# Optimization experiments

Hardware: AMD Instinct MI355X
Metric: run time of the kernel (lower is better)

The kernel has to match this reference:

```python
import jax, jax.numpy as jnp
import numpy as np

B, T, H, W, C = 2, 8, 64, 64, 192
WIN = (4, 8, 8)
SHIFT = (2, 4, 4)
HEADS = 6
HID = 4 * C
N = WIN[0] * WIN[1] * WIN[2]  # 256 tokens per window
CPB_HID = 512


def window_partition(x, win):
    b, t, h, w, c = x.shape
    x = x.reshape(b, t // win[0], win[0], h // win[1], win[1], w // win[2], win[2], c)
    x = x.transpose(0, 1, 3, 5, 2, 4, 6, 7)
    return x.reshape(-1, win[0] * win[1] * win[2], c)


def window_reverse(wins, win, b, t, h, w):
    x = wins.reshape(b, t // win[0], h // win[1], w // win[2], win[0], win[1], win[2], -1)
    x = x.transpose(0, 1, 4, 2, 5, 3, 6, 7)
    return x.reshape(b, t, h, w, -1)


def _rel_coords_table():
    axes = [np.arange(-(WIN[i] - 1), WIN[i], dtype=np.float32) for i in range(3)]
    tbl = np.stack(np.meshgrid(*axes, indexing='ij'), axis=-1)  # (2wt-1,2wh-1,2ww-1,3)
    for i in range(3):
        tbl[..., i] /= WIN[i] - 1
    tbl *= 8.0
    tbl = np.sign(tbl) * np.log2(np.abs(tbl) + 1.0) / np.log2(8.0)
    return tbl.reshape(-1, 3)


def _rel_pos_index():
    coords = np.stack(np.meshgrid(np.arange(WIN[0]), np.arange(WIN[1]), np.arange(WIN[2]), indexing='ij'))
    cf = coords.reshape(3, -1)
    rel = (cf[:, :, None] - cf[:, None, :]).transpose(1, 2, 0)
    rel[..., 0] += WIN[0] - 1
    rel[..., 1] += WIN[1] - 1
    rel[..., 2] += WIN[2] - 1
    rel[..., 0] *= (2 * WIN[1] - 1) * (2 * WIN[2] - 1)
    rel[..., 1] *= 2 * WIN[2] - 1
    return rel.sum(-1)  # (N, N) int


def _attn_mask():
    img = np.zeros((1, T, H, W, 1), dtype=np.float32)
    cnt = 0
    for d in (slice(-WIN[0]), slice(-WIN[0], -SHIFT[0]), slice(-SHIFT[0], None)):
        for h in (slice(-WIN[1]), slice(-WIN[1], -SHIFT[1]), slice(-SHIFT[1], None)):
            for w in (slice(-WIN[2]), slice(-WIN[2], -SHIFT[2]), slice(-SHIFT[2], None)):
                img[:, d, h, w, :] = cnt
                cnt += 1
    mw = window_partition(img, WIN).squeeze(-1)  # (nW, N)
    am = mw[:, None, :] - mw[:, :, None]
    return np.where(am != 0, -100.0, 0.0).astype(np.float32)


REL_TABLE = jnp.asarray(_rel_coords_table())      # (M, 3)
RPI = jnp.asarray(_rel_pos_index().reshape(-1))   # (N*N,)
MASK = jnp.asarray(_attn_mask())                  # (nW, N, N)


def _ln(x, g, b):
    m = x.mean(-1, keepdims=True)
    v = x.var(-1, keepdims=True)
    return (x - m) / jnp.sqrt(v + 1e-5) * g + b


def setup_inputs() -> dict:
    key = jax.random.key(0)
    ks = jax.random.split(key, 16)
    s = lambda fan: 1.0 / np.sqrt(fan)
    return {
        'x': jax.random.normal(ks[0], (B, T, H, W, C), jnp.float32),
        'qkv_w': jax.random.normal(ks[1], (3 * C, C), jnp.float32) * s(C),
        'qkv_b': jnp.zeros((3 * C,), jnp.float32),
        'proj_w': jax.random.normal(ks[2], (C, C), jnp.float32) * s(C),
        'proj_b': jnp.zeros((C,), jnp.float32),
        'cpb_w1': jax.random.normal(ks[3], (CPB_HID, 3), jnp.float32) * s(3),
        'cpb_b1': jnp.zeros((CPB_HID,), jnp.float32),
        'cpb_w2': jax.random.normal(ks[4], (HEADS, CPB_HID), jnp.float32) * s(CPB_HID),
        'logit_scale': jnp.log(10.0 * jnp.ones((HEADS, 1, 1), jnp.float32)),
        'norm1_g': jnp.ones((C,), jnp.float32),
        'norm1_b': jnp.zeros((C,), jnp.float32),
        'norm2_g': jnp.ones((C,), jnp.float32),
        'norm2_b': jnp.zeros((C,), jnp.float32),
        'fc1_w': jax.random.normal(ks[5], (HID, C), jnp.float32) * s(C),
        'fc1_b': jnp.zeros((HID,), jnp.float32),
        'fc2_w': jax.random.normal(ks[6], (C, HID), jnp.float32) * s(HID),
        'fc2_b': jnp.zeros((C,), jnp.float32),
    }


def reference(x, qkv_w, qkv_b, proj_w, proj_b, cpb_w1, cpb_b1, cpb_w2,
              logit_scale, norm1_g, norm1_b, norm2_g, norm2_b,
              fc1_w, fc1_b, fc2_w, fc2_b):
    shortcut = x
    # cyclic shift
    xs = jnp.roll(x, shift=(-SHIFT[0], -SHIFT[1], -SHIFT[2]), axis=(1, 2, 3))
    xw = window_partition(xs, WIN)  # (B*nW, N, C)
    B_ = xw.shape[0]
    d = C // HEADS
    qkv = (xw @ qkv_w.T + qkv_b).reshape(B_, N, 3, HEADS, d).transpose(2, 0, 3, 1, 4)
    q, k, v = qkv[0], qkv[1], qkv[2]  # (B_, h, N, d)
    # cosine attention (F.normalize eps=1e-12)
    qn = q / jnp.maximum(jnp.linalg.norm(q, axis=-1, keepdims=True), 1e-12)
    kn = k / jnp.maximum(jnp.linalg.norm(k, axis=-1, keepdims=True), 1e-12)
    attn = jnp.einsum('bhnd,bhmd->bhnm', qn, kn)
    scale = jnp.exp(jnp.minimum(logit_scale, jnp.log(100.0)))  # clamp at log(1/0.01)
    attn = attn * scale
    # continuous relative position bias
    tbl = jax.nn.relu(REL_TABLE @ cpb_w1.T + cpb_b1) @ cpb_w2.T  # (M, heads)
    bias = tbl[RPI].reshape(N, N, HEADS).transpose(2, 0, 1)      # (h, N, N)
    attn = attn + 16.0 * jax.nn.sigmoid(bias)[None]
    # shift mask
    nW = MASK.shape[0]
    attn = attn.reshape(B_ // nW, nW, HEADS, N, N) + MASK[None, :, None]
    attn = jax.nn.softmax(attn.reshape(B_, HEADS, N, N), axis=-1)
    out = jnp.einsum('bhnm,bhmd->bhnd', attn, v)
    out = out.transpose(0, 2, 1, 3).reshape(B_, N, C)
    out = out @ proj_w.T + proj_b
    xr = window_reverse(out, WIN, B, T, H, W)
    xr = jnp.roll(xr, shift=SHIFT, axis=(1, 2, 3))
    # SwinV2 res-post-norm residual
    x = shortcut + _ln(xr, norm1_g, norm1_b)
    h1 = jax.nn.gelu(x @ fc1_w.T + fc1_b, approximate=False)
    x = x + _ln(h1 @ fc2_w.T + fc2_b, norm2_g, norm2_b)
    return x
```

## Files before the change

### kernel.cpp

```cpp
#include <hip/hip_runtime.h>
#include <math.h>


typedef short short8 __attribute__((ext_vector_type(8)));
typedef short short4v __attribute__((ext_vector_type(4)));
typedef float f32x4 __attribute__((ext_vector_type(4)));

__device__ __forceinline__ short f2bf(float f) {
    union { float f; unsigned u; } v; v.f = f;
    unsigned r = v.u + 0x7FFF + ((v.u >> 16) & 1);
    return (short)(r >> 16);
}
__device__ __forceinline__ short f2h(float f) {
    _Float16 h = (_Float16)f;
    union { _Float16 h; short s; } u; u.h = h; return u.s;
}
__device__ __forceinline__ float h2f(short s) {
    union { _Float16 h; short s; } u; u.s = s; return (float)u.h;
}

__device__ __forceinline__ float gelu_fast(float x) {
    float s = x * x;
    float t = fmaf(0.044715f, s, 1.0f);
    float y = -1.5957691216057308f * x * t;
    return x * __builtin_amdgcn_rcpf(1.0f + __expf(y));
}

__global__ __launch_bounds__(64) void pack_w_k(const float* __restrict__ w,
                                               short* __restrict__ dst, int K) {
    int lane = threadIdx.x;
    int ktn = K >> 5;
    int nt = blockIdx.x / ktn, kt = blockIdx.x % ktn;
    int r = lane & 15, q = lane >> 4;
    const float* src = w + (size_t)(nt * 16 + r) * K + kt * 32 + q * 8;
    short8 v;
#pragma unroll
    for (int j = 0; j < 8; j++) v[j] = f2bf(src[j]);
    ((short8*)dst)[(size_t)blockIdx.x * 64 + lane] = v;
}

__global__ __launch_bounds__(64) void cpb_table_k(const float* __restrict__ w1,
                                                  const float* __restrict__ b1,
                                                  const float* __restrict__ w2,
                                                  float* __restrict__ tbl6) {
    int m = blockIdx.x;
    int lane = threadIdx.x;
    int it = m / 225;
    int ih = (m / 15) % 15;
    int iw = m % 15;
    float r0 = (float)(it - 3) * (8.0f / 3.0f);
    float r1 = (float)(ih - 7) * (8.0f / 7.0f);
    float r2 = (float)(iw - 7) * (8.0f / 7.0f);
    float c0 = (r0 < 0.f ? -1.f : 1.f) * log2f(fabsf(r0) + 1.0f) * (1.0f / 3.0f);
    float c1 = (r1 < 0.f ? -1.f : 1.f) * log2f(fabsf(r1) + 1.0f) * (1.0f / 3.0f);
    float c2 = (r2 < 0.f ? -1.f : 1.f) * log2f(fabsf(r2) + 1.0f) * (1.0f / 3.0f);
    float hv[8];
#pragma unroll
    for (int j = 0; j < 8; j++) {
        int t = lane * 8 + j;
        hv[j] = fmaxf(0.0f, c0 * w1[3 * t] + c1 * w1[3 * t + 1] + c2 * w1[3 * t + 2] + b1[t]);
    }
#pragma unroll
    for (int head = 0; head < 6; head++) {
        float s = 0.f;
#pragma unroll
        for (int j = 0; j < 8; j++) s += hv[j] * w2[head * 512 + lane * 8 + j];
        s += __shfl_xor(s, 1);
        s += __shfl_xor(s, 2);
        s += __shfl_xor(s, 4);
        s += __shfl_xor(s, 8);
        s += __shfl_xor(s, 16);
        s += __shfl_xor(s, 32);
        if (lane == 0) tbl6[m * 6 + head] = s;
    }
}

__global__ __launch_bounds__(256) void bias_k(const float* __restrict__ tbl6,
                                              short* __restrict__ biasPK) {
    int idx = blockIdx.x * 256 + threadIdx.x;
    int kh = idx & 1;
    int query = (idx >> 1) & 255;
    int r = (idx >> 9) & 15;
    int s = (idx >> 13) & 7;
    int h = idx >> 16;
    int key = s * 32 + kh * 16 + r;
    int dt = (query >> 6) - (key >> 6) + 3;
    int dh = ((query >> 3) & 7) - ((key >> 3) & 7) + 7;
    int dw = (query & 7) - (key & 7) + 7;
    int rel = dt * 225 + dh * 15 + dw;
    float v = tbl6[rel * 6 + h];
    biasPK[idx] = f2h(16.0f / (1.0f + expf(-v)));
}

#define ZSTR 388
__global__ __launch_bounds__(256) void qkv_mfma_k(const float* __restrict__ x,
                                                  const short* __restrict__ wqp,
                                                  const float* __restrict__ qkv_b,
                                                  short* __restrict__ qbf,
                                                  short* __restrict__ kbf,
                                                  short* __restrict__ vtb) {
    __shared__ float Z[32 * ZSTR];
    int tid = threadIdx.x, lane = tid & 63, w = tid >> 6;
    int r = lane & 15, q = lane >> 4;
    int b_ = blockIdx.x >> 3, n0 = (blockIdx.x & 7) << 5;
    int b = b_ >> 7, win = b_ & 127;
    int wt = win >> 6, wh = (win >> 3) & 7, ww = win & 7;

    short8 af[2][6];
#pragma unroll
    for (int m = 0; m < 2; m++) {
        int n = n0 + m * 16 + r;
        int t0 = ((wt * 4 + (n >> 6)) + 2) & 7;
        int h0 = ((wh * 8 + ((n >> 3) & 7)) + 4) & 63;
        int w0 = ((ww * 8 + (n & 7)) + 4) & 63;
        const float* src = x + ((size_t)((b * 8 + t0) * 64 + h0) * 64 + w0) * 192 + q * 8;
#pragma unroll
        for (int kt = 0; kt < 6; kt++) {
            float4 x0 = *(const float4*)(src + kt * 32);
            float4 x1 = *(const float4*)(src + kt * 32 + 4);
            short8 v;
            v[0] = f2bf(x0.x); v[1] = f2bf(x0.y); v[2] = f2bf(x0.z); v[3] = f2bf(x0.w);
            v[4] = f2bf(x1.x); v[5] = f2bf(x1.y); v[6] = f2bf(x1.z); v[7] = f2bf(x1.w);
            af[m][kt] = v;
        }
    }

    for (int ntl = 0; ntl < 9; ntl++) {
        int nt = w * 9 + ntl;
        float bias = qkv_b[nt * 16 + r];
        short8 bfr[6];
#pragma unroll
        for (int kt = 0; kt < 6; kt++)
            bfr[kt] = ((const short8*)wqp)[(size_t)(nt * 6 + kt) * 64 + lane];
        f32x4 a0 = {bias, bias, bias, bias};
        f32x4 a1 = {bias, bias, bias, bias};
#pragma unroll
        for (int kt = 0; kt < 6; kt++) {
            a0 = __builtin_amdgcn_mfma_f32_16x16x32_bf16(af[0][kt], bfr[kt], a0, 0, 0, 0);
            a1 = __builtin_amdgcn_mfma_f32_16x16x32_bf16(af[1][kt], bfr[kt], a1, 0, 0, 0);
        }
        int col = nt * 16 + r;
        if (nt < 24) {
#pragma unroll
            for (int reg = 0; reg < 4; reg++) {
                Z[(q * 4 + reg) * ZSTR + col] = a0[reg];
                Z[(16 + q * 4 + reg) * ZSTR + col] = a1[reg];
            }
        } else {
            int ch = col - 384;
            int hh = ch >> 5, dd = ch & 31;
            short* vb = vtb + ((size_t)(b_ * 6 + hh) * 32 + dd) * 256 + n0;
            short4v p0, p1;
#pragma unroll
            for (int reg = 0; reg < 4; reg++) { p0[reg] = f2bf(a0[reg]); p1[reg] = f2bf(a1[reg]); }
            *(short4v*)(vb + q * 4) = p0;
            *(short4v*)(vb + 16 + q * 4) = p1;
        }
    }
    __syncthreads();
    for (int rw = tid; rw < 384; rw += 256) {
        int token = rw / 12, rr = rw - token * 12;
        int isq = rr < 6 ? 1 : 0;
        int h = isq ? rr : rr - 6;
        const float* rp = &Z[token * ZSTR + rr * 32];
        float ss = 0.f;
#pragma unroll
        for (int d4 = 0; d4 < 8; d4++) {
            f32x4 v4 = *(const f32x4*)(rp + d4 * 4);
            ss += v4[0] * v4[0] + v4[1] * v4[1] + v4[2] * v4[2] + v4[3] * v4[3];
        }
        float inv = 1.0f / fmaxf(sqrtf(ss), 1e-12f);
        short* dst = (isq ? qbf : kbf) + ((size_t)(b_ * 6 + h) * 256 + n0 + token) * 32;
#pragma unroll
        for (int d8 = 0; d8 < 4; d8++) {
            f32x4 a4 = *(const f32x4*)(rp + d8 * 8);
            f32x4 b4 = *(const f32x4*)(rp + d8 * 8 + 4);
            short8 v;
            v[0] = f2bf(a4[0] * inv); v[1] = f2bf(a4[1] * inv);
            v[2] = f2bf(a4[2] * inv); v[3] = f2bf(a4[3] * inv);
            v[4] = f2bf(b4[0] * inv); v[5] = f2bf(b4[1] * inv);
            v[6] = f2bf(b4[2] * inv); v[7] = f2bf(b4[3] * inv);
            *(short8*)(dst + d8 * 8) = v;
        }
    }
}

#define KSTR 40
#define VSTR 264
#define PSTR 40
__global__ __launch_bounds__(256) void attn_mfma_k(const short* __restrict__ qbf,
                                                   const short* __restrict__ kbf,
                                                   const short* __restrict__ vtb,
                                                   const short* __restrict__ biasPK,
                                                   const float* __restrict__ logit_scale,
                                                   short* __restrict__ att) {
    __shared__ short Ks[256 * KSTR];
    __shared__ short Vs[32 * VSTR];
    __shared__ short Ps[4][16 * PSTR];
    int tid = threadIdx.x, lane = tid & 63, w = tid >> 6;
    int r = lane & 15, q = lane >> 4;
    int b_ = blockIdx.x / 6, h = blockIdx.x % 6;
    size_t base = (size_t)(b_ * 6 + h) * 8192;

    const short8* kg = (const short8*)(kbf + base);
    const short8* vg = (const short8*)(vtb + base);
    for (int i = tid; i < 1024; i += 256) {
        short8 kv = kg[i];
        *(short8*)&Ks[(i >> 2) * KSTR + (i & 3) * 8] = kv;
        short8 vv = vg[i];
        *(short8*)&Vs[(i >> 5) * VSTR + (i & 31) * 8] = vv;
    }

    short8 qf[4];
#pragma unroll
    for (int mt = 0; mt < 4; mt++)
        qf[mt] = *(const short8*)(qbf + base + (size_t)(w * 64 + mt * 16 + r) * 32 + q * 8);

    float scale = __expf(fminf(logit_scale[h], 4.6051702f));
    float M = scale + 16.0f;
    int win = b_ & 127;
    int wt4 = (win >> 6) * 4, wh8 = ((win >> 3) & 7) * 8, ww8 = (win & 7) * 8;
    auto region = [&](int n) {
        int ts = wt4 + (n >> 6), hs = wh8 + ((n >> 3) & 7), wsv = ww8 + (n & 7);
        int rt = ts < 4 ? 0 : (ts < 6 ? 1 : 2);
        int rh = hs < 56 ? 0 : (hs < 60 ? 1 : 2);
        int rw = wsv < 56 ? 0 : (wsv < 60 ? 1 : 2);
        return rt * 9 + rh * 3 + rw;
    };
    int rowreg[4][4];
#pragma unroll
    for (int mt = 0; mt < 4; mt++)
#pragma unroll
        for (int reg = 0; reg < 4; reg++)
            rowreg[mt][reg] = region(w * 64 + mt * 16 + q * 4 + reg);

    f32x4 O[4][2];
    float lp[4][4];
#pragma unroll
    for (int mt = 0; mt < 4; mt++) {
        O[mt][0] = (f32x4){0.f, 0.f, 0.f, 0.f};
        O[mt][1] = (f32x4){0.f, 0.f, 0.f, 0.f};
#pragma unroll
        for (int reg = 0; reg < 4; reg++) lp[mt][reg] = 0.f;
    }
    __syncthreads();

    const short* bh = biasPK + ((size_t)h << 16);
    for (int s = 0; s < 8; s++) {
        short8 kf0 = *(const short8*)&Ks[(s * 32 + r) * KSTR + q * 8];
        short8 kf1 = *(const short8*)&Ks[(s * 32 + 16 + r) * KSTR + q * 8];
        short8 vf0 = *(const short8*)&Vs[r * VSTR + s * 32 + q * 8];
        short8 vf1 = *(const short8*)&Vs[(16 + r) * VSTR + s * 32 + q * 8];
        int cr0 = region(s * 32 + r);
        int cr1 = region(s * 32 + 16 + r);
#pragma unroll
        for (int mt = 0; mt < 4; mt++) {
            f32x4 s0 = {0.f, 0.f, 0.f, 0.f};
            f32x4 s1 = {0.f, 0.f, 0.f, 0.f};
            s0 = __builtin_amdgcn_mfma_f32_16x16x32_bf16(qf[mt], kf0, s0, 0, 0, 0);
            s1 = __builtin_amdgcn_mfma_f32_16x16x32_bf16(qf[mt], kf1, s1, 0, 0, 0);
            int qcol = w * 64 + mt * 16 + q * 4;
            short8 bv = *(const short8*)(bh + (size_t)(s * 16 + r) * 512 + qcol * 2);
#pragma unroll
            for (int reg = 0; reg < 4; reg++) {
                float bb0 = h2f(bv[2 * reg]);
                float bb1 = h2f(bv[2 * reg + 1]);
                float v0 = s0[reg] * scale + bb0 + (cr0 == rowreg[mt][reg] ? 0.f : -100.f) - M;
                float v1 = s1[reg] * scale + bb1 + (cr1 == rowreg[mt][reg] ? 0.f : -100.f) - M;
                float p0 = __expf(v0);
                float p1 = __expf(v1);
                lp[mt][reg] += p0 + p1;
                Ps[w][(q * 4 + reg) * PSTR + r] = f2bf(p0);
                Ps[w][(q * 4 + reg) * PSTR + 16 + r] = f2bf(p1);
            }
            short8 pa = *(const short8*)&Ps[w][r * PSTR + q * 8];
            O[mt][0] = __builtin_amdgcn_mfma_f32_16x16x32_bf16(vf0, pa, O[mt][0], 0, 0, 0);
            O[mt][1] = __builtin_amdgcn_mfma_f32_16x16x32_bf16(vf1, pa, O[mt][1], 0, 0, 0);
        }
    }

#pragma unroll
    for (int mt = 0; mt < 4; mt++)
#pragma unroll
        for (int reg = 0; reg < 4; reg++) {
            float v = lp[mt][reg];
            v += __shfl_xor(v, 1);
            v += __shfl_xor(v, 2);
            v += __shfl_xor(v, 4);
            v += __shfl_xor(v, 8);
            lp[mt][reg] = 1.0f / v;
        }
#pragma unroll
    for (int mt = 0; mt < 4; mt++) {
        int srcl = (r >> 2) << 4;
        float t0 = __shfl(lp[mt][0], srcl);
        float t1 = __shfl(lp[mt][1], srcl);
        float t2 = __shfl(lp[mt][2], srcl);
        float t3 = __shfl(lp[mt][3], srcl);
        int rm = r & 3;
        float linv = rm == 0 ? t0 : (rm == 1 ? t1 : (rm == 2 ? t2 : t3));
        int query = w * 64 + mt * 16 + r;
        short* dst = att + ((size_t)b_ * 256 + query) * 192 + h * 32 + q * 4;
#pragma unroll
        for (int nt = 0; nt < 2; nt++) {
            short4v pv;
#pragma unroll
            for (int reg = 0; reg < 4; reg++) pv[reg] = f2bf(O[mt][nt][reg] * linv);
            *(short4v*)(dst + nt * 16) = pv;
        }
    }
}

__global__ __launch_bounds__(256) void proj_mfma_k(const short* __restrict__ att,
                                                   const short* __restrict__ wpp,
                                                   const float* __restrict__ proj_b,
                                                   const float* __restrict__ x,
                                                   const float* __restrict__ g1,
                                                   const float* __restrict__ b1n,
                                                   float* __restrict__ out,
                                                   short* __restrict__ xmb) {
    __shared__ float ps[32][4], pss[32][4];
    __shared__ float mean_s[32], inv_s[32];
    int tid = threadIdx.x, lane = tid & 63, w = tid >> 6;
    int r = lane & 15, q = lane >> 4;
    int b_ = blockIdx.x >> 3, n0 = (blockIdx.x & 7) << 5;

    short8 af[2][6];
#pragma unroll
    for (int m = 0; m < 2; m++) {
        const short* src = att + ((size_t)b_ * 256 + n0 + m * 16 + r) * 192 + q * 8;
#pragma unroll
        for (int kt = 0; kt < 6; kt++)
            af[m][kt] = *(const short8*)(src + kt * 32);
    }
    f32x4 acc[3][2];
#pragma unroll
    for (int ntl = 0; ntl < 3; ntl++) {
        int nt = w * 3 + ntl;
        f32x4 binit = *(const f32x4*)(proj_b + nt * 16 + q * 4);
        short8 bfr[6];
#pragma unroll
        for (int kt = 0; kt < 6; kt++)
            bfr[kt] = ((const short8*)wpp)[(size_t)(nt * 6 + kt) * 64 + lane];
        f32x4 a0 = binit, a1 = binit;
#pragma unroll
        for (int kt = 0; kt < 6; kt++) {
            a0 = __builtin_amdgcn_mfma_f32_16x16x32_bf16(bfr[kt], af[0][kt], a0, 0, 0, 0);
            a1 = __builtin_amdgcn_mfma_f32_16x16x32_bf16(bfr[kt], af[1][kt], a1, 0, 0, 0);
        }
        acc[ntl][0] = a0;
        acc[ntl][1] = a1;
    }
    float s0 = 0.f, ss0 = 0.f, s1 = 0.f, ss1 = 0.f;
#pragma unroll
    for (int ntl = 0; ntl < 3; ntl++)
#pragma unroll
        for (int reg = 0; reg < 4; reg++) {
            float z0 = acc[ntl][0][reg], z1 = acc[ntl][1][reg];
            s0 += z0; ss0 += z0 * z0;
            s1 += z1; ss1 += z1 * z1;
        }
    s0 += __shfl_xor(s0, 16); ss0 += __shfl_xor(ss0, 16);
    s0 += __shfl_xor(s0, 32); ss0 += __shfl_xor(ss0, 32);
    s1 += __shfl_xor(s1, 16); ss1 += __shfl_xor(ss1, 16);
    s1 += __shfl_xor(s1, 32); ss1 += __shfl_xor(ss1, 32);
    if (q == 0) {
        ps[r][w] = s0;  pss[r][w] = ss0;
        ps[16 + r][w] = s1;  pss[16 + r][w] = ss1;
    }
    __syncthreads();
    if (tid < 32) {
        float sm = ps[tid][0] + ps[tid][1] + ps[tid][2] + ps[tid][3];
        float sq = pss[tid][0] + pss[tid][1] + pss[tid][2] + pss[tid][3];
        float mean = sm * (1.0f / 192.0f);
        float var = sq * (1.0f / 192.0f) - mean * mean;
        mean_s[tid] = mean;
        inv_s[tid] = 1.0f / sqrtf(var + 1e-5f);
    }
    __syncthreads();
    int b = b_ >> 7, win = b_ & 127;
    int wt = win >> 6, wh = (win >> 3) & 7, ww = win & 7;
#pragma unroll
    for (int mh = 0; mh < 2; mh++) {
        int token = mh * 16 + r;
        int n = n0 + token;
        int t0 = ((wt * 4 + (n >> 6)) + 2) & 7;
        int h0 = ((wh * 8 + ((n >> 3) & 7)) + 4) & 63;
        int w0 = ((ww * 8 + (n & 7)) + 4) & 63;
        size_t gb = ((size_t)((b * 8 + t0) * 64 + h0) * 64 + w0) * 192;
        float mean = mean_s[token], inv = inv_s[token];
#pragma unroll
        for (int ntl = 0; ntl < 3; ntl++) {
            int ch = (w * 3 + ntl) * 16 + q * 4;
            f32x4 zv = acc[ntl][mh];
            f32x4 gv = *(const f32x4*)(g1 + ch);
            f32x4 bv = *(const f32x4*)(b1n + ch);
            f32x4 xv = *(const f32x4*)(x + gb + ch);
            f32x4 o;
            short4v xm;
#pragma unroll
            for (int j = 0; j < 4; j++) {
                o[j] = xv[j] + (zv[j] - mean) * inv * gv[j] + bv[j];
                xm[j] = f2bf(o[j]);
            }
            *(f32x4*)(out + gb + ch) = o;
            *(short4v*)(xmb + gb + ch) = xm;
        }
    }
}

#define XSTR 204
#define H2STR 268
__global__ __launch_bounds__(512, 4) void mlp_mfma_k(const short* __restrict__ xmb,
                                                     const short* __restrict__ w1p,
                                                     const short* __restrict__ w2p,
                                                     const float* __restrict__ fc1_b,
                                                     const float* __restrict__ fc2_b,
                                                     const float* __restrict__ g2,
                                                     const float* __restrict__ b2,
                                                     float* __restrict__ out) {
    __shared__ short Xs[64 * XSTR];
    __shared__ short Hs[64 * H2STR];
    __shared__ float ps[64][4], pss[64][4];
    __shared__ float mean_s[64], inv_s[64];
    int tid = threadIdx.x;
    int lane = tid & 63, w = tid >> 6;
    int r = lane & 15, q = lane >> 4;
    size_t tok0 = (size_t)blockIdx.x * 64;

    for (int i = tid; i < 1536; i += 512) {
        int token = i / 24, ch8 = (i - token * 24) * 8;
        short8 v = *(const short8*)(xmb + (tok0 + token) * 192 + ch8);
        *(short8*)&Xs[token * XSTR + ch8] = v;
    }
    __syncthreads();

    int mg = w >> 2;
    int ng = w & 3;
    f32x4 acc2[6];
#pragma unroll
    for (int i = 0; i < 6; i++) acc2[i] = (f32x4){0.f, 0.f, 0.f, 0.f};

    for (int c = 0; c < 3; c++) {
        {
            int ntg0 = c * 16 + 2 * w;
            f32x4 a[2][4];
#pragma unroll
            for (int ntl = 0; ntl < 2; ntl++) {
                f32x4 binit = *(const f32x4*)(fc1_b + (ntg0 + ntl) * 16 + q * 4);
#pragma unroll
                for (int m = 0; m < 4; m++) a[ntl][m] = binit;
            }
#pragma unroll
            for (int kt = 0; kt < 6; kt++) {
                short8 w0 = ((const short8*)w1p)[(size_t)((ntg0) * 6 + kt) * 64 + lane];
                short8 w1f = ((const short8*)w1p)[(size_t)((ntg0 + 1) * 6 + kt) * 64 + lane];
                short8 xb[4];
#pragma unroll
                for (int m = 0; m < 4; m++)
                    xb[m] = *(const short8*)&Xs[(m * 16 + r) * XSTR + kt * 32 + q * 8];
#pragma unroll
                for (int m = 0; m < 4; m++) {
                    a[0][m] = __builtin_amdgcn_mfma_f32_16x16x32_bf16(w0, xb[m], a[0][m], 0, 0, 0);
                    a[1][m] = __builtin_amdgcn_mfma_f32_16x16x32_bf16(w1f, xb[m], a[1][m], 0, 0, 0);
                }
            }
#pragma unroll
            for (int ntl = 0; ntl < 2; ntl++) {
                int hcol = (2 * w + ntl) * 16 + q * 4;
#pragma unroll
                for (int m = 0; m < 4; m++) {
                    short4v p;
#pragma unroll
                    for (int reg = 0; reg < 4; reg++) p[reg] = f2bf(gelu_fast(a[ntl][m][reg]));
                    *(short4v*)&Hs[(m * 16 + r) * H2STR + hcol] = p;
                }
            }
        }
        __syncthreads();

#pragma unroll
        for (int kk = 0; kk < 8; kk++) {
            short8 hb0 = *(const short8*)&Hs[((mg * 2) * 16 + r) * H2STR + kk * 32 + q * 8];
            short8 hb1 = *(const short8*)&Hs[((mg * 2 + 1) * 16 + r) * H2STR + kk * 32 + q * 8];
            int kkg = c * 8 + kk;
#pragma unroll
            for (int n = 0; n < 3; n++) {
                int ntz = ng * 3 + n;
                short8 wf = ((const short8*)w2p)[(size_t)(ntz * 24 + kkg) * 64 + lane];
                acc2[n * 2 + 0] = __builtin_amdgcn_mfma_f32_16x16x32_bf16(wf, hb0, acc2[n * 2 + 0], 0, 0, 0);
                acc2[n * 2 + 1] = __builtin_amdgcn_mfma_f32_16x16x32_bf16(wf, hb1, acc2[n * 2 + 1], 0, 0, 0);
            }
        }
        __syncthreads();
    }

    float s0 = 0.f, ss0 = 0.f, s1 = 0.f, ss1 = 0.f;
#pragma unroll
    for (int n = 0; n < 3; n++) {
        f32x4 b4 = *(const f32x4*)(fc2_b + (ng * 3 + n) * 16 + q * 4);
        f32x4 z0 = acc2[n * 2 + 0] + b4;
        f32x4 z1 = acc2[n * 2 + 1] + b4;
        acc2[n * 2 + 0] = z0;
        acc2[n * 2 + 1] = z1;
#pragma unroll
        for (int reg = 0; reg < 4; reg++) {
            s0 += z0[reg]; ss0 += z0[reg] * z0[reg];
            s1 += z1[reg]; ss1 += z1[reg] * z1[reg];
        }
    }
    s0 += __shfl_xor(s0, 16); ss0 += __shfl_xor(ss0, 16);
    s0 += __shfl_xor(s0, 32); ss0 += __shfl_xor(ss0, 32);
    s1 += __shfl_xor(s1, 16); ss1 += __shfl_xor(ss1, 16);
    s1 += __shfl_xor(s1, 32); ss1 += __shfl_xor(ss1, 32);
    if (q == 0) {
        int t0 = mg * 32 + r;
        ps[t0][ng] = s0;  pss[t0][ng] = ss0;
        ps[t0 + 16][ng] = s1;  pss[t0 + 16][ng] = ss1;
    }
    __syncthreads();
    if (tid < 64) {
        float sm = ps[tid][0] + ps[tid][1] + ps[tid][2] + ps[tid][3];
        float sq = pss[tid][0] + pss[tid][1] + pss[tid][2] + pss[tid][3];
        float mean = sm * (1.0f / 192.0f);
        float var = sq * (1.0f / 192.0f) - mean * mean;
        mean_s[tid] = mean;
        inv_s[tid] = 1.0f / sqrtf(var + 1e-5f);
    }
    __syncthreads();
#pragma unroll
    for (int n = 0; n < 3; n++) {
        int ntz = ng * 3 + n;
        f32x4 g4 = *(const f32x4*)(g2 + ntz * 16 + q * 4);
        f32x4 bb4 = *(const f32x4*)(b2 + ntz * 16 + q * 4);
#pragma unroll
        for (int mh = 0; mh < 2; mh++) {
            int token = mg * 32 + mh * 16 + r;
            float mean = mean_s[token], inv = inv_s[token];
            size_t gi = (tok0 + token) * 192 + ntz * 16 + q * 4;
            f32x4 o = *(const f32x4*)(out + gi);
            f32x4 z = acc2[n * 2 + mh];
            f32x4 res;
#pragma unroll
            for (int reg = 0; reg < 4; reg++)
                res[reg] = o[reg] + (z[reg] - mean) * inv * g4[reg] + bb4[reg];
            *(f32x4*)(out + gi) = res;
        }
    }
}

extern "C" void kernel_launch(void* const* d_in, const int* in_sizes, int n_in,
                              void* d_out, int out_size, void* d_ws, size_t ws_size,
                              hipStream_t stream) {
    const float* x           = (const float*)d_in[0];
    const float* qkv_w       = (const float*)d_in[1];
    const float* qkv_b       = (const float*)d_in[2];
    const float* proj_w      = (const float*)d_in[3];
    const float* proj_b      = (const float*)d_in[4];
    const float* cpb_w1      = (const float*)d_in[5];
    const float* cpb_b1      = (const float*)d_in[6];
    const float* cpb_w2      = (const float*)d_in[7];
    const float* logit_scale = (const float*)d_in[8];
    const float* norm1_g     = (const float*)d_in[9];
    const float* norm1_b     = (const float*)d_in[10];
    const float* norm2_g     = (const float*)d_in[11];
    const float* norm2_b     = (const float*)d_in[12];
    const float* fc1_w       = (const float*)d_in[13];
    const float* fc1_b       = (const float*)d_in[14];
    const float* fc2_w       = (const float*)d_in[15];
    const float* fc2_b       = (const float*)d_in[16];
    float* out = (float*)d_out;

    float* ws = (float*)d_ws;
    const size_t QKVE = (size_t)256 * 6 * 256 * 32;
    short* att    = (short*)ws;
    short* biasPK = (short*)(ws + QKVE);
    float* tbl6   = ws + QKVE + (size_t)6 * 256 * 256;
    short* w1pack = (short*)(tbl6 + 9472);
    short* w2pack = w1pack + (size_t)768 * 192;
    short* wqpack = w2pack + (size_t)192 * 768;
    short* wppack = wqpack + (size_t)576 * 192;
    short* qbf    = wppack + (size_t)192 * 192;
    short* kbf    = qbf + QKVE;
    short* vtb    = kbf + QKVE;
    short* xmb    = vtb + QKVE;

    hipLaunchKernelGGL(pack_w_k, dim3(288), dim3(64), 0, stream, fc1_w, w1pack, 192);
    hipLaunchKernelGGL(pack_w_k, dim3(288), dim3(64), 0, stream, fc2_w, w2pack, 768);
    hipLaunchKernelGGL(pack_w_k, dim3(216), dim3(64), 0, stream, qkv_w, wqpack, 192);
    hipLaunchKernelGGL(pack_w_k, dim3(72), dim3(64), 0, stream, proj_w, wppack, 192);
    hipLaunchKernelGGL(cpb_table_k, dim3(1575), dim3(64), 0, stream, cpb_w1, cpb_b1, cpb_w2, tbl6);
    hipLaunchKernelGGL(bias_k, dim3(1536), dim3(256), 0, stream, tbl6, biasPK);
    hipLaunchKernelGGL(qkv_mfma_k, dim3(2048), dim3(256), 0, stream, x, wqpack, qkv_b, qbf, kbf, vtb);
    hipLaunchKernelGGL(attn_mfma_k, dim3(1536), dim3(256), 0, stream, qbf, kbf, vtb, biasPK, logit_scale, att);
    hipLaunchKernelGGL(proj_mfma_k, dim3(2048), dim3(256), 0, stream, att, wppack, proj_b, x, norm1_g, norm1_b, out, xmb);
    hipLaunchKernelGGL(mlp_mfma_k, dim3(1024), dim3(512), 0, stream, xmb, w1pack, w2pack,
                       fc1_b, fc2_b, norm2_g, norm2_b, out);
}
```

Before: 367.7 us.

## Compute transposed attention scores and pass probabilities via shuffles instead of LDS

The attention kernel now computes S^T (keys as rows) by swapping the MFMA operands and feeds the bf16-packed probabilities to the PV MFMA through lane shuffles, dropping the per-wave LDS round trip for P. The bias table is re-laid out query-major so each lane does one contiguous 16-byte load, and the shift-mask region checks are computed per key block from precomputed components. The row-sum reduction is simplified to two xor shuffles. Separately, the MLP kernel's LDS row strides are changed, which may alter bank-conflict behaviour.

```diff
diff --git a/kernel.cpp b/kernel.cpp
--- a/kernel.cpp
+++ b/kernel.cpp
@@ -10,6 +10,9 @@
     union { float f; unsigned u; } v; v.f = f;
     unsigned r = v.u + 0x7FFF + ((v.u >> 16) & 1);
     return (short)(r >> 16);
+}
+__device__ __forceinline__ unsigned pk2bf(float lo, float hi) {
+    return ((unsigned)(unsigned short)f2bf(lo)) | (((unsigned)(unsigned short)f2bf(hi)) << 16);
 }
 __device__ __forceinline__ short f2h(float f) {
     _Float16 h = (_Float16)f;
@@ -76,20 +79,20 @@
 }
 
 __global__ __launch_bounds__(256) void bias_k(const float* __restrict__ tbl6,
-                                              short* __restrict__ biasPK) {
+                                              short* __restrict__ biasQK) {
     int idx = blockIdx.x * 256 + threadIdx.x;
     int kh = idx & 1;
-    int query = (idx >> 1) & 255;
-    int r = (idx >> 9) & 15;
-    int s = (idx >> 13) & 7;
+    int key_lo = (idx >> 1) & 15;
+    int s = (idx >> 5) & 7;
+    int query = (idx >> 8) & 255;
     int h = idx >> 16;
-    int key = s * 32 + kh * 16 + r;
+    int key = s * 32 + kh * 16 + key_lo;
     int dt = (query >> 6) - (key >> 6) + 3;
     int dh = ((query >> 3) & 7) - ((key >> 3) & 7) + 7;
     int dw = (query & 7) - (key & 7) + 7;
     int rel = dt * 225 + dh * 15 + dw;
     float v = tbl6[rel * 6 + h];
-    biasPK[idx] = f2h(16.0f / (1.0f + expf(-v)));
+    biasQK[idx] = f2h(16.0f / (1.0f + expf(-v)));
 }
 
 #define ZSTR 388
@@ -187,16 +190,14 @@
 
 #define KSTR 40
 #define VSTR 264
-#define PSTR 40
 __global__ __launch_bounds__(256) void attn_mfma_k(const short* __restrict__ qbf,
                                                    const short* __restrict__ kbf,
                                                    const short* __restrict__ vtb,
-                                                   const short* __restrict__ biasPK,
+                                                   const short* __restrict__ biasQK,
                                                    const float* __restrict__ logit_scale,
                                                    short* __restrict__ att) {
     __shared__ short Ks[256 * KSTR];
     __shared__ short Vs[32 * VSTR];
-    __shared__ short Ps[4][16 * PSTR];
     int tid = threadIdx.x, lane = tid & 63, w = tid >> 6;
     int r = lane & 15, q = lane >> 4;
     int b_ = blockIdx.x / 6, h = blockIdx.x % 6;
@@ -227,78 +228,103 @@
         int rw = wsv < 56 ? 0 : (wsv < 60 ? 1 : 2);
         return rt * 9 + rh * 3 + rw;
     };
-    int rowreg[4][4];
-#pragma unroll
-    for (int mt = 0; mt < 4; mt++)
-#pragma unroll
-        for (int reg = 0; reg < 4; reg++)
-            rowreg[mt][reg] = region(w * 64 + mt * 16 + q * 4 + reg);
+    int qreg[4];
+#pragma unroll
+    for (int mt = 0; mt < 4; mt++) qreg[mt] = region(w * 64 + mt * 16 + r);
+    int rw4[4];
+#pragma unroll
+    for (int reg = 0; reg < 4; reg++) {
+        int wsv = ww8 + (q & 1) * 4 + reg;
+        rw4[reg] = wsv < 56 ? 0 : (wsv < 60 ? 1 : 2);
+    }
 
     f32x4 O[4][2];
-    float lp[4][4];
+    float lpv[4];
 #pragma unroll
     for (int mt = 0; mt < 4; mt++) {
         O[mt][0] = (f32x4){0.f, 0.f, 0.f, 0.f};
         O[mt][1] = (f32x4){0.f, 0.f, 0.f, 0.f};
-#pragma unroll
-        for (int reg = 0; reg < 4; reg++) lp[mt][reg] = 0.f;
+        lpv[mt] = 0.f;
     }
     __syncthreads();
 
-    const short* bh = biasPK + ((size_t)h << 16);
+    int qa = 2 * (q & 1);
+    int srcA = (qa << 4) | r;
+    int srcB = ((qa + 1) << 4) | r;
+    bool loSel = q < 2;
+
+    const short* bh = biasQK + ((size_t)h << 16);
     for (int s = 0; s < 8; s++) {
         short8 kf0 = *(const short8*)&Ks[(s * 32 + r) * KSTR + q * 8];
         short8 kf1 = *(const short8*)&Ks[(s * 32 + 16 + r) * KSTR + q * 8];
         short8 vf0 = *(const short8*)&Vs[r * VSTR + s * 32 + q * 8];
         short8 vf1 = *(const short8*)&Vs[(16 + r) * VSTR + s * 32 + q * 8];
-        int cr0 = region(s * 32 + r);
-        int cr1 = region(s * 32 + 16 + r);
+        int ts = wt4 + (s >> 1);
+        int rt_s = (ts < 4 ? 0 : (ts < 6 ? 1 : 2)) * 9;
+        int hs0 = wh8 + (s & 1) * 4 + (q >> 1);
+        int hs1 = hs0 + 2;
+        int rh0 = (hs0 < 56 ? 0 : (hs0 < 60 ? 1 : 2)) * 3;
+        int rh1 = (hs1 < 56 ? 0 : (hs1 < 60 ? 1 : 2)) * 3;
+        int kreg0[4], kreg1[4];
+#pragma unroll
+        for (int reg = 0; reg < 4; reg++) {
+            kreg0[reg] = rt_s + rh0 + rw4[reg];
+            kreg1[reg] = rt_s + rh1 + rw4[reg];
+        }
 #pragma unroll
         for (int mt = 0; mt < 4; mt++) {
             f32x4 s0 = {0.f, 0.f, 0.f, 0.f};
             f32x4 s1 = {0.f, 0.f, 0.f, 0.f};
-            s0 = __builtin_amdgcn_mfma_f32_16x16x32_bf16(qf[mt], kf0, s0, 0, 0, 0);
-            s1 = __builtin_amdgcn_mfma_f32_16x16x32_bf16(qf[mt], kf1, s1, 0, 0, 0);
-            int qcol = w * 64 + mt * 16 + q * 4;
-            short8 bv = *(const short8*)(bh + (size_t)(s * 16 + r) * 512 + qcol * 2);
+            s0 = __builtin_amdgcn_mfma_f32_16x16x32_bf16(kf0, qf[mt], s0, 0, 0, 0);
+            s1 = __builtin_amdgcn_mfma_f32_16x16x32_bf16(kf1, qf[mt], s1, 0, 0, 0);
+            int query = w * 64 + mt * 16 + r;
+            short8 bv = *(const short8*)(bh + (size_t)query * 256 + s * 32 + q * 8);
+            float p0[4], p1[4];
+            float lsum = 0.f;
 #pragma unroll
             for (int reg = 0; reg < 4; reg++) {
                 float bb0 = h2f(bv[2 * reg]);
                 float bb1 = h2f(bv[2 * reg + 1]);
-                float v0 = s0[reg] * scale + bb0 + (cr0 == rowreg[mt][reg] ? 0.f : -100.f) - M;
-                float v1 = s1[reg] * scale + bb1 + (cr1 == rowreg[mt][reg] ? 0.f : -100.f) - M;
-                float p0 = __expf(v0);
-                float p1 = __expf(v1);
-                lp[mt][reg] += p0 + p1;
-                Ps[w][(q * 4 + reg) * PSTR + r] = f2bf(p0);
-                Ps[w][(q * 4 + reg) * PSTR + 16 + r] = f2bf(p1);
+                float v0 = s0[reg] * scale + bb0 + (kreg0[reg] == qreg[mt] ? 0.f : -100.f) - M;
+                float v1 = s1[reg] * scale + bb1 + (kreg1[reg] == qreg[mt] ? 0.f : -100.f) - M;
+                p0[reg] = __expf(v0);
+                p1[reg] = __expf(v1);
+                lsum += p0[reg] + p1[reg];
             }
-            short8 pa = *(const short8*)&Ps[w][r * PSTR + q * 8];
-            O[mt][0] = __builtin_amdgcn_mfma_f32_16x16x32_bf16(vf0, pa, O[mt][0], 0, 0, 0);
-            O[mt][1] = __builtin_amdgcn_mfma_f32_16x16x32_bf16(vf1, pa, O[mt][1], 0, 0, 0);
-        }
-    }
-
-#pragma unroll
-    for (int mt = 0; mt < 4; mt++)
-#pragma unroll
-        for (int reg = 0; reg < 4; reg++) {
-            float v = lp[mt][reg];
-            v += __shfl_xor(v, 1);
-            v += __shfl_xor(v, 2);
-            v += __shfl_xor(v, 4);
-            v += __shfl_xor(v, 8);
-            lp[mt][reg] = 1.0f / v;
-        }
+            lpv[mt] += lsum;
+            unsigned lo0 = pk2bf(p0[0], p0[1]);
+            unsigned lo1 = pk2bf(p0[2], p0[3]);
+            unsigned hi0 = pk2bf(p1[0], p1[1]);
+            unsigned hi1 = pk2bf(p1[2], p1[3]);
+            unsigned a0 = __shfl((int)lo0, srcA);
+            unsigned a1 = __shfl((int)lo1, srcA);
+            unsigned a2 = __shfl((int)lo0, srcB);
+            unsigned a3 = __shfl((int)lo1, srcB);
+            unsigned b0 = __shfl((int)hi0, srcA);
+            unsigned b1 = __shfl((int)hi1, srcA);
+            unsigned b2 = __shfl((int)hi0, srcB);
+            unsigned b3 = __shfl((int)hi1, srcB);
+            union { unsigned u[4]; short8 s8; } pu;
+            pu.u[0] = loSel ? a0 : b0;
+            pu.u[1] = loSel ? a1 : b1;
+            pu.u[2] = loSel ? a2 : b2;
+            pu.u[3] = loSel ? a3 : b3;
+            short8 pb = pu.s8;
+            O[mt][0] = __builtin_amdgcn_mfma_f32_16x16x32_bf16(vf0, pb, O[mt][0], 0, 0, 0);
+            O[mt][1] = __builtin_amdgcn_mfma_f32_16x16x32_bf16(vf1, pb, O[mt][1], 0, 0, 0);
+        }
+    }
+
 #pragma unroll
     for (int mt = 0; mt < 4; mt++) {
-        int srcl = (r >> 2) << 4;
-        float t0 = __shfl(lp[mt][0], srcl);
-        float t1 = __shfl(lp[mt][1], srcl);
-        float t2 = __shfl(lp[mt][2], srcl);
-        float t3 = __shfl(lp[mt][3], srcl);
-        int rm = r & 3;
-        float linv = rm == 0 ? t0 : (rm == 1 ? t1 : (rm == 2 ? t2 : t3));
+        float v = lpv[mt];
+        v += __shfl_xor(v, 16);
+        v += __shfl_xor(v, 32);
+        lpv[mt] = 1.0f / v;
+    }
+#pragma unroll
+    for (int mt = 0; mt < 4; mt++) {
+        float linv = lpv[mt];
         int query = w * 64 + mt * 16 + r;
         short* dst = att + ((size_t)b_ * 256 + query) * 192 + h * 32 + q * 4;
 #pragma unroll
@@ -409,8 +435,8 @@
     }
 }
 
-#define XSTR 204
-#define H2STR 268
+#define XSTR 200
+#define H2STR 264
 __global__ __launch_bounds__(512, 4) void mlp_mfma_k(const short* __restrict__ xmb,
                                                      const short* __restrict__ w1p,
                                                      const short* __restrict__ w2p,
@@ -574,7 +600,7 @@
     float* ws = (float*)d_ws;
     const size_t QKVE = (size_t)256 * 6 * 256 * 32;
     short* att    = (short*)ws;
-    short* biasPK = (short*)(ws + QKVE);
+    short* biasQK = (short*)(ws + QKVE);
     float* tbl6   = ws + QKVE + (size_t)6 * 256 * 256;
     short* w1pack = (short*)(tbl6 + 9472);
     short* w2pack = w1pack + (size_t)768 * 192;
@@ -590,9 +616,9 @@
     hipLaunchKernelGGL(pack_w_k, dim3(216), dim3(64), 0, stream, qkv_w, wqpack, 192);
     hipLaunchKernelGGL(pack_w_k, dim3(72), dim3(64), 0, stream, proj_w, wppack, 192);
     hipLaunchKernelGGL(cpb_table_k, dim3(1575), dim3(64), 0, stream, cpb_w1, cpb_b1, cpb_w2, tbl6);
-    hipLaunchKernelGGL(bias_k, dim3(1536), dim3(256), 0, stream, tbl6, biasPK);
+    hipLaunchKernelGGL(bias_k, dim3(1536), dim3(256), 0, stream, tbl6, biasQK);
     hipLaunchKernelGGL(qkv_mfma_k, dim3(2048), dim3(256), 0, stream, x, wqpack, qkv_b, qbf, kbf, vtb);
-    hipLaunchKernelGGL(attn_mfma_k, dim3(1536), dim3(256), 0, stream, qbf, kbf, vtb, biasPK, logit_scale, att);
+    hipLaunchKernelGGL(attn_mfma_k, dim3(1536), dim3(256), 0, stream, qbf, kbf, vtb, biasQK, logit_scale, att);
     hipLaunchKernelGGL(proj_mfma_k, dim3(2048), dim3(256), 0, stream, att, wppack, proj_b, x, norm1_g, norm1_b, out, xmb);
     hipLaunchKernelGGL(mlp_mfma_k, dim3(1024), dim3(512), 0, stream, xmb, w1pack, w2pack,
                        fc1_b, fc2_b, norm2_g, norm2_b, out);
```

Result: no change. 364.4 us (-0.9%).
